# Kernel optimization log

Measured on AMD Instinct MI355X. Metric: run time of the kernel, lower is better.

## Reference

```python
import jax, jax.numpy as jnp
import numpy as np

N = 200000      # n_edges (1-simplices)
NNZ = 2000000   # nonzeros per sparse Laplacian
F_IN = 64       # num_edge_feats
F_H = 32        # f_size (hard-coded in FlowSAN)
F_OUT = 8       # output_size
G = 256         # number of graphs in batch
NEG_SLOPE = 0.2 # GAT LeakyReLU slope


def setup_inputs() -> dict:
    key = jax.random.key(0)
    ks = iter(jax.random.split(key, 64))

    def rn(shape, s=0.1):
        return jax.random.normal(next(ks), shape, dtype=jnp.float32) * s

    d = {"x1": jax.random.normal(next(ks), (N, F_IN), dtype=jnp.float32)}
    dims = [(F_IN, F_H), (F_H, F_H), (F_H, F_H), (F_H, F_OUT)]
    for i, (fi, fo) in enumerate(dims, 1):
        d[f"pW{i}"] = rn((fi, fo))                      # SANLayer.p_layer weight (bias=False)
        d[f"uW{i}"] = rn((fi, fo))                      # l_u GAT linear
        d[f"ua_s{i}"] = rn((fo,)); d[f"ua_d{i}"] = rn((fo,))  # l_u GAT attention vec halves
        d[f"dW{i}"] = rn((fi, fo))                      # l_d GAT linear
        d[f"da_s{i}"] = rn((fo,)); d[f"da_d{i}"] = rn((fo,))
    d["l1_idx"] = jax.random.randint(next(ks), (2, NNZ), 0, N, dtype=jnp.int32)
    d["l1_val"] = jax.random.normal(next(ks), (NNZ,), dtype=jnp.float32)
    d["lu_idx"] = jax.random.randint(next(ks), (2, NNZ), 0, N, dtype=jnp.int32)
    d["ld_idx"] = jax.random.randint(next(ks), (2, NNZ), 0, N, dtype=jnp.int32)
    d["batch1"] = jnp.sort(jax.random.randint(next(ks), (N,), 0, G, dtype=jnp.int32))
    return d


def _gat(x, W, a_s, a_d, idx):
    # GAT-style attention over the nonzero pattern of the sparse Laplacian
    h = x @ W                                   # [N, fo]
    row, col = idx[0], idx[1]
    e = jax.nn.leaky_relu(h[row] @ a_s + h[col] @ a_d, NEG_SLOPE)  # [nnz]
    e = e - jax.ops.segment_max(e, row, num_segments=N)[row]       # stable softmax
    w = jnp.exp(e)
    alpha = w / (jax.ops.segment_sum(w, row, num_segments=N)[row] + 1e-16)
    return jax.ops.segment_sum(alpha[:, None] * h[col], row, num_segments=N)


def _san(x, pW, uW, ua_s, ua_d, dW, da_s, da_d, l1_idx, l1_val, lu_idx, ld_idx):
    # p branch: torch.sparse.mm(L1, x @ pW)
    hp = x @ pW
    row, col = l1_idx[0], l1_idx[1]
    hp = jax.ops.segment_sum(l1_val[:, None] * hp[col], row, num_segments=N)
    hu = _gat(x, uW, ua_s, ua_d, lu_idx)
    hd = _gat(x, dW, da_s, da_d, ld_idx)
    return hu + hd + hp


def reference(x1,
              pW1, uW1, ua_s1, ua_d1, dW1, da_s1, da_d1,
              pW2, uW2, ua_s2, ua_d2, dW2, da_s2, da_d2,
              pW3, uW3, ua_s3, ua_d3, dW3, da_s3, da_d3,
              pW4, uW4, ua_s4, ua_d4, dW4, da_s4, da_d4,
              l1_idx, l1_val, lu_idx, ld_idx, batch1):
    layers = [
        (pW1, uW1, ua_s1, ua_d1, dW1, da_s1, da_d1),
        (pW2, uW2, ua_s2, ua_d2, dW2, da_s2, da_d2),
        (pW3, uW3, ua_s3, ua_d3, dW3, da_s3, da_d3),
        (pW4, uW4, ua_s4, ua_d4, dW4, da_s4, da_d4),
    ]
    x = x1
    for p in layers:
        x = jax.nn.relu(_san(x, *p, l1_idx, l1_val, lu_idx, ld_idx))
    # global_mean_pool(|x|, batch1)
    cnt = jax.ops.segment_sum(jnp.ones((N,), jnp.float32), batch1, num_segments=G)
    pooled = jax.ops.segment_sum(jnp.abs(x), batch1, num_segments=G) / jnp.maximum(cnt, 1.0)[:, None]
    return jax.nn.softmax(pooled, axis=1)
```

## Files before the change

### kernel.cpp

```cpp
#include <hip/hip_runtime.h>
#include <cmath>


#define N_    200000
#define NNZ_  2000000
#define G_    256


__global__ __launch_bounds__(256) void hist_k(const int* __restrict__ lu, const int* __restrict__ ld,
                                              const int* __restrict__ l1, int* __restrict__ deg,
                                              int* __restrict__ tick) {
    int i = blockIdx.x * 256 + threadIdx.x;
    if (i >= NNZ_ / 4) return;
    int e = i * 4;
    int4 ru = *reinterpret_cast<const int4*>(lu + e);
    int4 rd = *reinterpret_cast<const int4*>(ld + e);
    int4 rl = *reinterpret_cast<const int4*>(l1 + e);
    int4 t;
    t.x = atomicAdd(&deg[ru.x], 1);
    t.y = atomicAdd(&deg[ru.y], 1);
    t.z = atomicAdd(&deg[ru.z], 1);
    t.w = atomicAdd(&deg[ru.w], 1);
    *reinterpret_cast<int4*>(tick + e) = t;
    t.x = atomicAdd(&deg[N_ + rd.x], 1);
    t.y = atomicAdd(&deg[N_ + rd.y], 1);
    t.z = atomicAdd(&deg[N_ + rd.z], 1);
    t.w = atomicAdd(&deg[N_ + rd.w], 1);
    *reinterpret_cast<int4*>(tick + NNZ_ + e) = t;
    t.x = atomicAdd(&deg[2 * N_ + rl.x], 1);
    t.y = atomicAdd(&deg[2 * N_ + rl.y], 1);
    t.z = atomicAdd(&deg[2 * N_ + rl.z], 1);
    t.w = atomicAdd(&deg[2 * N_ + rl.w], 1);
    *reinterpret_cast<int4*>(tick + 2 * NNZ_ + e) = t;
}

__global__ __launch_bounds__(256) void scan1_k(const int* __restrict__ in, int* __restrict__ out,
                                               int* __restrict__ bsum, int n) {
    __shared__ int lds[256];
    int tid = threadIdx.x;
    int base = blockIdx.x * 1024 + tid * 4;
    int v0 = (base + 0 < n) ? in[base + 0] : 0;
    int v1 = (base + 1 < n) ? in[base + 1] : 0;
    int v2 = (base + 2 < n) ? in[base + 2] : 0;
    int v3 = (base + 3 < n) ? in[base + 3] : 0;
    int s = v0 + v1 + v2 + v3;
    lds[tid] = s;
    __syncthreads();
    for (int off = 1; off < 256; off <<= 1) {
        int t = (tid >= off) ? lds[tid - off] : 0;
        __syncthreads();
        lds[tid] += t;
        __syncthreads();
    }
    int excl = lds[tid] - s;
    if (base + 0 < n) out[base + 0] = excl;
    if (base + 1 < n) out[base + 1] = excl + v0;
    if (base + 2 < n) out[base + 2] = excl + v0 + v1;
    if (base + 3 < n) out[base + 3] = excl + v0 + v1 + v2;
    if (tid == 255) bsum[blockIdx.x] = lds[255];
}

__global__ __launch_bounds__(256) void scan2_k(int* __restrict__ bsum, int nb, int* __restrict__ total_out) {
    __shared__ int lds[256];
    __shared__ int run_s;
    int tid = threadIdx.x;
    if (tid == 0) run_s = 0;
    __syncthreads();
    for (int c0 = 0; c0 < nb; c0 += 256) {
        int i = c0 + tid;
        int s = (i < nb) ? bsum[i] : 0;
        lds[tid] = s;
        __syncthreads();
        for (int off = 1; off < 256; off <<= 1) {
            int t = (tid >= off) ? lds[tid - off] : 0;
            __syncthreads();
            lds[tid] += t;
            __syncthreads();
        }
        int run = run_s;
        if (i < nb) bsum[i] = run + lds[tid] - s;
        __syncthreads();
        if (tid == 0) run_s = run + lds[255];
        __syncthreads();
    }
    if (tid == 0 && total_out) *total_out = run_s;
}

__global__ __launch_bounds__(256) void scan3_k(int* __restrict__ out, const int* __restrict__ bsum, int n) {
    int add = bsum[blockIdx.x];
    int base = blockIdx.x * 1024 + threadIdx.x * 4;
    #pragma unroll
    for (int k = 0; k < 4; ++k)
        if (base + k < n) out[base + k] += add;
}

__global__ __launch_bounds__(256) void scatter_k(const int* __restrict__ lu, const int* __restrict__ ld,
                                                 const int* __restrict__ l1, const float* __restrict__ l1v,
                                                 const int* __restrict__ rptr, const int* __restrict__ tick,
                                                 int* __restrict__ cols, float* __restrict__ vcsr) {
    int i = blockIdx.x * 256 + threadIdx.x;
    if (i >= NNZ_ / 4) return;
    int e = i * 4;
    {
        int4 r = *reinterpret_cast<const int4*>(lu + e);
        int4 c = *reinterpret_cast<const int4*>(lu + NNZ_ + e);
        int4 t = *reinterpret_cast<const int4*>(tick + e);
        __builtin_nontemporal_store(c.x, &cols[rptr[r.x] + t.x]);
        __builtin_nontemporal_store(c.y, &cols[rptr[r.y] + t.y]);
        __builtin_nontemporal_store(c.z, &cols[rptr[r.z] + t.z]);
        __builtin_nontemporal_store(c.w, &cols[rptr[r.w] + t.w]);
    }
    {
        int4 r = *reinterpret_cast<const int4*>(ld + e);
        int4 c = *reinterpret_cast<const int4*>(ld + NNZ_ + e);
        int4 t = *reinterpret_cast<const int4*>(tick + NNZ_ + e);
        __builtin_nontemporal_store(c.x, &cols[rptr[N_ + r.x] + t.x]);
        __builtin_nontemporal_store(c.y, &cols[rptr[N_ + r.y] + t.y]);
        __builtin_nontemporal_store(c.z, &cols[rptr[N_ + r.z] + t.z]);
        __builtin_nontemporal_store(c.w, &cols[rptr[N_ + r.w] + t.w]);
    }
    {
        int4 r = *reinterpret_cast<const int4*>(l1 + e);
        int4 c = *reinterpret_cast<const int4*>(l1 + NNZ_ + e);
        int4 t = *reinterpret_cast<const int4*>(tick + 2 * NNZ_ + e);
        float4 v = *reinterpret_cast<const float4*>(l1v + e);
        int p0 = rptr[2 * N_ + r.x] + t.x;
        int p1 = rptr[2 * N_ + r.y] + t.y;
        int p2 = rptr[2 * N_ + r.z] + t.z;
        int p3 = rptr[2 * N_ + r.w] + t.w;
        __builtin_nontemporal_store(c.x, &cols[p0]);
        __builtin_nontemporal_store(c.y, &cols[p1]);
        __builtin_nontemporal_store(c.z, &cols[p2]);
        __builtin_nontemporal_store(c.w, &cols[p3]);
        __builtin_nontemporal_store(v.x, &vcsr[p0 - 2 * NNZ_]);
        __builtin_nontemporal_store(v.y, &vcsr[p1 - 2 * NNZ_]);
        __builtin_nontemporal_store(v.z, &vcsr[p2 - 2 * NNZ_]);
        __builtin_nontemporal_store(v.w, &vcsr[p3 - 2 * NNZ_]);
    }
}


template <int FI, int FO>
__global__ __launch_bounds__(256) void gemm3_k(const float* __restrict__ x,
                                               const float* __restrict__ uW, const float* __restrict__ uas,
                                               const float* __restrict__ uad,
                                               const float* __restrict__ dW, const float* __restrict__ das,
                                               const float* __restrict__ dad,
                                               const float* __restrict__ pW,
                                               float* __restrict__ HU, float* __restrict__ HD,
                                               float* __restrict__ HP,
                                               float* __restrict__ ssu, float* __restrict__ sdu,
                                               float* __restrict__ ssd, float* __restrict__ sdd) {
    constexpr int ROWS = 256 / FO;
    constexpr int XS = FI + 1;
    __shared__ float Wu[FI * FO], Wd[FI * FO], Wp[FI * FO];
    __shared__ float xs[ROWS * XS];
    int tid = threadIdx.x;
    for (int i = tid; i < FI * FO; i += 256) {
        Wu[i] = uW[i];
        Wd[i] = dW[i];
        Wp[i] = pW[i];
    }
    int row0 = blockIdx.x * ROWS;
    for (int i = tid; i < ROWS * FI; i += 256) {
        int r = i / FI, k = i - r * FI;
        int gr = row0 + r;
        xs[r * XS + k] = (gr < N_) ? x[(size_t)gr * FI + k] : 0.f;
    }
    __syncthreads();
    int r = tid / FO, j = tid - (tid / FO) * FO;
    int grow = row0 + r;
    float au = 0.f, ad = 0.f, ap = 0.f;
    #pragma unroll
    for (int k = 0; k < FI; ++k) {
        float xv = xs[r * XS + k];
        au = fmaf(xv, Wu[k * FO + j], au);
        ad = fmaf(xv, Wd[k * FO + j], ad);
        ap = fmaf(xv, Wp[k * FO + j], ap);
    }
    if (grow < N_) {
        HU[(size_t)grow * FO + j] = au;
        HD[(size_t)grow * FO + j] = ad;
        HP[(size_t)grow * FO + j] = ap;
    }
    float vsu = au * uas[j], vdu = au * uad[j];
    float vsd = ad * das[j], vdd = ad * dad[j];
    #pragma unroll
    for (int m = FO / 2; m >= 1; m >>= 1) {
        vsu += __shfl_xor(vsu, m, FO);
        vdu += __shfl_xor(vdu, m, FO);
        vsd += __shfl_xor(vsd, m, FO);
        vdd += __shfl_xor(vdd, m, FO);
    }
    if (j == 0 && grow < N_) {
        ssu[grow] = vsu; sdu[grow] = vdu;
        ssd[grow] = vsd; sdd[grow] = vdd;
    }
}


template <int FO, bool GAT>
__device__ __forceinline__ void edge_loop(const int* __restrict__ cols, const float* __restrict__ sdv,
                                          const float* __restrict__ vals, const float* __restrict__ H,
                                          int b, int e, int lane, float s_row, int vbase,
                                          float& ax, float& ay, float& az, float& aw, float& z) {
    int p = b;
    for (; p + 4 <= e; p += 4) {
        int c0 = cols[p], c1 = cols[p + 1], c2 = cols[p + 2], c3 = cols[p + 3];
        const float4 h0 = *reinterpret_cast<const float4*>(H + (size_t)c0 * FO + lane * 4);
        const float4 h1 = *reinterpret_cast<const float4*>(H + (size_t)c1 * FO + lane * 4);
        const float4 h2 = *reinterpret_cast<const float4*>(H + (size_t)c2 * FO + lane * 4);
        const float4 h3 = *reinterpret_cast<const float4*>(H + (size_t)c3 * FO + lane * 4);
        float w0, w1, w2, w3;
        if constexpr (GAT) {
            float g0 = s_row + sdv[c0];
            float g1 = s_row + sdv[c1];
            float g2 = s_row + sdv[c2];
            float g3 = s_row + sdv[c3];
            g0 = g0 > 0.f ? g0 : 0.2f * g0;
            g1 = g1 > 0.f ? g1 : 0.2f * g1;
            g2 = g2 > 0.f ? g2 : 0.2f * g2;
            g3 = g3 > 0.f ? g3 : 0.2f * g3;
            w0 = __expf(g0); w1 = __expf(g1); w2 = __expf(g2); w3 = __expf(g3);
            z += (w0 + w1) + (w2 + w3);
        } else {
            w0 = vals[p - vbase];
            w1 = vals[p - vbase + 1];
            w2 = vals[p - vbase + 2];
            w3 = vals[p - vbase + 3];
        }
        ax = fmaf(w0, h0.x, ax); ay = fmaf(w0, h0.y, ay);
        az = fmaf(w0, h0.z, az); aw = fmaf(w0, h0.w, aw);
        ax = fmaf(w1, h1.x, ax); ay = fmaf(w1, h1.y, ay);
        az = fmaf(w1, h1.z, az); aw = fmaf(w1, h1.w, aw);
        ax = fmaf(w2, h2.x, ax); ay = fmaf(w2, h2.y, ay);
        az = fmaf(w2, h2.z, az); aw = fmaf(w2, h2.w, aw);
        ax = fmaf(w3, h3.x, ax); ay = fmaf(w3, h3.y, ay);
        az = fmaf(w3, h3.z, az); aw = fmaf(w3, h3.w, aw);
    }
    for (; p < e; ++p) {
        int c = cols[p];
        const float4 hv = *reinterpret_cast<const float4*>(H + (size_t)c * FO + lane * 4);
        float wv;
        if constexpr (GAT) {
            float g = s_row + sdv[c];
            g = g > 0.f ? g : 0.2f * g;
            wv = __expf(g);
            z += wv;
        } else {
            wv = vals[p - vbase];
        }
        ax = fmaf(wv, hv.x, ax); ay = fmaf(wv, hv.y, ay);
        az = fmaf(wv, hv.z, az); aw = fmaf(wv, hv.w, aw);
    }
}

template <int FO>
__global__ __launch_bounds__(256) void gather3_k(const int* __restrict__ rptr, const int* __restrict__ cols,
                                                 const float* __restrict__ vcsr,
                                                 const float* __restrict__ HU, const float* __restrict__ HD,
                                                 const float* __restrict__ HP,
                                                 const float* __restrict__ ssu, const float* __restrict__ sdu,
                                                 const float* __restrict__ ssd, const float* __restrict__ sdd,
                                                 float* __restrict__ xout) {
    constexpr int LPR = FO / 4;
    constexpr int RPB = 256 / LPR;
    int tid = threadIdx.x;
    int lane = tid % LPR;
    int r = blockIdx.x * RPB + tid / LPR;
    if (r >= N_) return;
    float ox, oy, oz, ow;
    {
        float ax = 0.f, ay = 0.f, az = 0.f, aw = 0.f, z = 0.f;
        edge_loop<FO, true>(cols, sdu, nullptr, HU, rptr[r], rptr[r + 1], lane, ssu[r], 0,
                            ax, ay, az, aw, z);
        float inv = 1.f / (z + 1e-16f);
        ox = ax * inv; oy = ay * inv; oz = az * inv; ow = aw * inv;
    }
    {
        float ax = 0.f, ay = 0.f, az = 0.f, aw = 0.f, z = 0.f;
        edge_loop<FO, true>(cols, sdd, nullptr, HD, rptr[N_ + r], rptr[N_ + r + 1], lane, ssd[r], 0,
                            ax, ay, az, aw, z);
        float inv = 1.f / (z + 1e-16f);
        ox = fmaf(ax, inv, ox); oy = fmaf(ay, inv, oy);
        oz = fmaf(az, inv, oz); ow = fmaf(aw, inv, ow);
    }
    {
        float ax = 0.f, ay = 0.f, az = 0.f, aw = 0.f, z = 0.f;
        edge_loop<FO, false>(cols, nullptr, vcsr, HP, rptr[2 * N_ + r], rptr[2 * N_ + r + 1], lane,
                             0.f, 2 * NNZ_, ax, ay, az, aw, z);
        ox += ax; oy += ay; oz += az; ow += aw;
    }
    ox = fmaxf(ox, 0.f); oy = fmaxf(oy, 0.f);
    oz = fmaxf(oz, 0.f); ow = fmaxf(ow, 0.f);
    *reinterpret_cast<float4*>(xout + (size_t)r * FO + lane * 4) = make_float4(ox, oy, oz, ow);
}


__global__ __launch_bounds__(256) void pool_k(const float* __restrict__ x, const int* __restrict__ batch,
                                              float* __restrict__ out) {
    int g = blockIdx.x;
    __shared__ float part[256];
    __shared__ int sse[2];
    if (threadIdx.x < 2) {
        int target = g + threadIdx.x;
        int lo = 0, hi = N_;
        while (lo < hi) {
            int mid = (lo + hi) >> 1;
            if (batch[mid] < target) lo = mid + 1; else hi = mid;
        }
        sse[threadIdx.x] = lo;
    }
    __syncthreads();
    int s = sse[0], e = sse[1];
    int f = threadIdx.x % 8;
    float acc = 0.f;
    for (int i = s + threadIdx.x / 8; i < e; i += 32) acc += fabsf(x[(size_t)i * 8 + f]);
    part[threadIdx.x] = acc;
    __syncthreads();
    if (threadIdx.x < 8) {
        float t = 0.f;
        #pragma unroll
        for (int k = 0; k < 32; ++k) t += part[k * 8 + f];
        float cnt = (float)(e - s);
        part[f] = t / fmaxf(cnt, 1.0f);
    }
    __syncthreads();
    if (threadIdx.x == 0) {
        float m = part[0];
        for (int j = 1; j < 8; ++j) m = fmaxf(m, part[j]);
        float zs = 0.f;
        float ex[8];
        for (int j = 0; j < 8; ++j) { ex[j] = __expf(part[j] - m); zs += ex[j]; }
        for (int j = 0; j < 8; ++j) out[g * 8 + j] = ex[j] / zs;
    }
}


template <int FI, int FO>
static void run_layer(const float* xin, float* xout, const float* const* W,
                      float* HU, float* HD, float* HP,
                      float* SSU, float* SDU, float* SSD, float* SDD,
                      const int* PTR, const int* COLS, const float* VCSR, hipStream_t stream) {
    constexpr int ROWS = 256 / FO;
    constexpr int RPB = 256 / (FO / 4);
    gemm3_k<FI, FO><<<(N_ + ROWS - 1) / ROWS, 256, 0, stream>>>(
        xin, W[1], W[2], W[3], W[4], W[5], W[6], W[0],
        HU, HD, HP, SSU, SDU, SSD, SDD);
    gather3_k<FO><<<(N_ + RPB - 1) / RPB, 256, 0, stream>>>(
        PTR, COLS, VCSR, HU, HD, HP, SSU, SDU, SSD, SDD, xout);
}

extern "C" void kernel_launch(void* const* d_in, const int* in_sizes, int n_in, void* d_out,
                              int out_size, void* d_ws, size_t ws_size, hipStream_t stream) {
    (void)in_sizes; (void)n_in; (void)out_size; (void)ws_size;
    const float* x1     = (const float*)d_in[0];
    const int*   l1_idx = (const int*)d_in[29];
    const float* l1_val = (const float*)d_in[30];
    const int*   lu_idx = (const int*)d_in[31];
    const int*   ld_idx = (const int*)d_in[32];
    const int*   batch1 = (const int*)d_in[33];
    float* out = (float*)d_out;

    char* w = (char*)d_ws;
    size_t off = 0;
    auto alloc = [&](size_t bytes) -> char* {
        char* p = w + off;
        off = (off + bytes + 255) & ~(size_t)255;
        return p;
    };
    float* X    = (float*)alloc((size_t)N_ * 32 * 4);
    float* HU   = (float*)alloc((size_t)N_ * 32 * 4);
    float* HD   = (float*)alloc((size_t)N_ * 32 * 4);
    float* HP   = (float*)alloc((size_t)N_ * 32 * 4);
    float* SSU  = (float*)alloc((size_t)N_ * 4);
    float* SDU  = (float*)alloc((size_t)N_ * 4);
    float* SSD  = (float*)alloc((size_t)N_ * 4);
    float* SDD  = (float*)alloc((size_t)N_ * 4);
    int*   PTR  = (int*)alloc((size_t)(3 * N_ + 1) * 4);
    int*   DEG  = (int*)alloc((size_t)3 * N_ * 4);
    int*   BSUM = (int*)alloc((size_t)1024 * 4);
    int*   TICK = (int*)alloc((size_t)3 * NNZ_ * 4);
    int*   COLS = (int*)alloc((size_t)3 * NNZ_ * 4);
    float* VCSR = (float*)alloc((size_t)NNZ_ * 4);

    hipMemsetAsync(DEG, 0, (size_t)3 * N_ * 4, stream);
    int qbl = (NNZ_ / 4 + 255) / 256;
    hist_k<<<qbl, 256, 0, stream>>>(lu_idx, ld_idx, l1_idx, DEG, TICK);
    int n3 = 3 * N_;
    int nb = (n3 + 1023) / 1024;
    scan1_k<<<nb, 256, 0, stream>>>(DEG, PTR, BSUM, n3);
    scan2_k<<<1, 256, 0, stream>>>(BSUM, nb, PTR + n3);
    scan3_k<<<nb, 256, 0, stream>>>(PTR, BSUM, n3);
    scatter_k<<<qbl, 256, 0, stream>>>(lu_idx, ld_idx, l1_idx, l1_val, PTR, TICK, COLS, VCSR);

    const float* W0[7] = {(const float*)d_in[1], (const float*)d_in[2], (const float*)d_in[3],
                          (const float*)d_in[4], (const float*)d_in[5], (const float*)d_in[6],
                          (const float*)d_in[7]};
    const float* W1[7] = {(const float*)d_in[8],  (const float*)d_in[9],  (const float*)d_in[10],
                          (const float*)d_in[11], (const float*)d_in[12], (const float*)d_in[13],
                          (const float*)d_in[14]};
    const float* W2[7] = {(const float*)d_in[15], (const float*)d_in[16], (const float*)d_in[17],
                          (const float*)d_in[18], (const float*)d_in[19], (const float*)d_in[20],
                          (const float*)d_in[21]};
    const float* W3[7] = {(const float*)d_in[22], (const float*)d_in[23], (const float*)d_in[24],
                          (const float*)d_in[25], (const float*)d_in[26], (const float*)d_in[27],
                          (const float*)d_in[28]};

    run_layer<64, 32>(x1, X, W0, HU, HD, HP, SSU, SDU, SSD, SDD, PTR, COLS, VCSR, stream);
    run_layer<32, 32>(X, X, W1, HU, HD, HP, SSU, SDU, SSD, SDD, PTR, COLS, VCSR, stream);
    run_layer<32, 32>(X, X, W2, HU, HD, HP, SSU, SDU, SSD, SDD, PTR, COLS, VCSR, stream);
    run_layer<32, 8>(X, X, W3, HU, HD, HP, SSU, SDU, SSD, SDD, PTR, COLS, VCSR, stream);

    pool_k<<<G_, 256, 0, stream>>>(X, batch1, out);
}
```

Baseline: 1.552 ms.

## Fuse CSR scatter with layer-1 GEMM and split gather rows across two teams

```diff
diff --git a/kernel.cpp b/kernel.cpp
--- a/kernel.cpp
+++ b/kernel.cpp
@@ -94,48 +94,102 @@
         if (base + k < n) out[base + k] += add;
 }
 
-__global__ __launch_bounds__(256) void scatter_k(const int* __restrict__ lu, const int* __restrict__ ld,
-                                                 const int* __restrict__ l1, const float* __restrict__ l1v,
-                                                 const int* __restrict__ rptr, const int* __restrict__ tick,
-                                                 int* __restrict__ cols, float* __restrict__ vcsr) {
-    int i = blockIdx.x * 256 + threadIdx.x;
-    if (i >= NNZ_ / 4) return;
-    int e = i * 4;
-    {
-        int4 r = *reinterpret_cast<const int4*>(lu + e);
-        int4 c = *reinterpret_cast<const int4*>(lu + NNZ_ + e);
-        int4 t = *reinterpret_cast<const int4*>(tick + e);
-        __builtin_nontemporal_store(c.x, &cols[rptr[r.x] + t.x]);
-        __builtin_nontemporal_store(c.y, &cols[rptr[r.y] + t.y]);
-        __builtin_nontemporal_store(c.z, &cols[rptr[r.z] + t.z]);
-        __builtin_nontemporal_store(c.w, &cols[rptr[r.w] + t.w]);
-    }
-    {
-        int4 r = *reinterpret_cast<const int4*>(ld + e);
-        int4 c = *reinterpret_cast<const int4*>(ld + NNZ_ + e);
-        int4 t = *reinterpret_cast<const int4*>(tick + NNZ_ + e);
-        __builtin_nontemporal_store(c.x, &cols[rptr[N_ + r.x] + t.x]);
-        __builtin_nontemporal_store(c.y, &cols[rptr[N_ + r.y] + t.y]);
-        __builtin_nontemporal_store(c.z, &cols[rptr[N_ + r.z] + t.z]);
-        __builtin_nontemporal_store(c.w, &cols[rptr[N_ + r.w] + t.w]);
-    }
-    {
-        int4 r = *reinterpret_cast<const int4*>(l1 + e);
-        int4 c = *reinterpret_cast<const int4*>(l1 + NNZ_ + e);
-        int4 t = *reinterpret_cast<const int4*>(tick + 2 * NNZ_ + e);
+
+template <int FI, int FO, int SCB>
+__global__ __launch_bounds__(256) void scat_gemm_k(
+    const int* __restrict__ lu, const int* __restrict__ ld, const int* __restrict__ l1,
+    const float* __restrict__ l1v, const int* __restrict__ rptr, const int* __restrict__ tick,
+    int* __restrict__ cols, float* __restrict__ vcsr,
+    const float* __restrict__ x,
+    const float* __restrict__ uW, const float* __restrict__ uas, const float* __restrict__ uad,
+    const float* __restrict__ dW, const float* __restrict__ das, const float* __restrict__ dad,
+    const float* __restrict__ pW,
+    float* __restrict__ HU, float* __restrict__ HD, float* __restrict__ HP,
+    float* __restrict__ ssu, float* __restrict__ sdu,
+    float* __restrict__ ssd, float* __restrict__ sdd) {
+    if (blockIdx.x < SCB) {
+        int i = blockIdx.x * 256 + threadIdx.x;
+        if (i >= NNZ_ / 4) return;
+        int e = i * 4;
+        int4 ru = *reinterpret_cast<const int4*>(lu + e);
+        int4 rd = *reinterpret_cast<const int4*>(ld + e);
+        int4 rl = *reinterpret_cast<const int4*>(l1 + e);
+        int4 cu = *reinterpret_cast<const int4*>(lu + NNZ_ + e);
+        int4 cd = *reinterpret_cast<const int4*>(ld + NNZ_ + e);
+        int4 cl = *reinterpret_cast<const int4*>(l1 + NNZ_ + e);
+        int4 tu = *reinterpret_cast<const int4*>(tick + e);
+        int4 td = *reinterpret_cast<const int4*>(tick + NNZ_ + e);
+        int4 tl = *reinterpret_cast<const int4*>(tick + 2 * NNZ_ + e);
         float4 v = *reinterpret_cast<const float4*>(l1v + e);
-        int p0 = rptr[2 * N_ + r.x] + t.x;
-        int p1 = rptr[2 * N_ + r.y] + t.y;
-        int p2 = rptr[2 * N_ + r.z] + t.z;
-        int p3 = rptr[2 * N_ + r.w] + t.w;
-        __builtin_nontemporal_store(c.x, &cols[p0]);
-        __builtin_nontemporal_store(c.y, &cols[p1]);
-        __builtin_nontemporal_store(c.z, &cols[p2]);
-        __builtin_nontemporal_store(c.w, &cols[p3]);
-        __builtin_nontemporal_store(v.x, &vcsr[p0 - 2 * NNZ_]);
-        __builtin_nontemporal_store(v.y, &vcsr[p1 - 2 * NNZ_]);
-        __builtin_nontemporal_store(v.z, &vcsr[p2 - 2 * NNZ_]);
-        __builtin_nontemporal_store(v.w, &vcsr[p3 - 2 * NNZ_]);
+        int pu0 = rptr[ru.x] + tu.x, pu1 = rptr[ru.y] + tu.y;
+        int pu2 = rptr[ru.z] + tu.z, pu3 = rptr[ru.w] + tu.w;
+        int pd0 = rptr[N_ + rd.x] + td.x, pd1 = rptr[N_ + rd.y] + td.y;
+        int pd2 = rptr[N_ + rd.z] + td.z, pd3 = rptr[N_ + rd.w] + td.w;
+        int pl0 = rptr[2 * N_ + rl.x] + tl.x, pl1 = rptr[2 * N_ + rl.y] + tl.y;
+        int pl2 = rptr[2 * N_ + rl.z] + tl.z, pl3 = rptr[2 * N_ + rl.w] + tl.w;
+        __builtin_nontemporal_store(cu.x, &cols[pu0]);
+        __builtin_nontemporal_store(cu.y, &cols[pu1]);
+        __builtin_nontemporal_store(cu.z, &cols[pu2]);
+        __builtin_nontemporal_store(cu.w, &cols[pu3]);
+        __builtin_nontemporal_store(cd.x, &cols[pd0]);
+        __builtin_nontemporal_store(cd.y, &cols[pd1]);
+        __builtin_nontemporal_store(cd.z, &cols[pd2]);
+        __builtin_nontemporal_store(cd.w, &cols[pd3]);
+        __builtin_nontemporal_store(cl.x, &cols[pl0]);
+        __builtin_nontemporal_store(cl.y, &cols[pl1]);
+        __builtin_nontemporal_store(cl.z, &cols[pl2]);
+        __builtin_nontemporal_store(cl.w, &cols[pl3]);
+        __builtin_nontemporal_store(v.x, &vcsr[pl0 - 2 * NNZ_]);
+        __builtin_nontemporal_store(v.y, &vcsr[pl1 - 2 * NNZ_]);
+        __builtin_nontemporal_store(v.z, &vcsr[pl2 - 2 * NNZ_]);
+        __builtin_nontemporal_store(v.w, &vcsr[pl3 - 2 * NNZ_]);
+        return;
+    }
+    int bid = blockIdx.x - SCB;
+    constexpr int ROWS = 256 / FO;
+    constexpr int XS = FI + 1;
+    __shared__ float Wu[FI * FO], Wd[FI * FO], Wp[FI * FO];
+    __shared__ float xs[ROWS * XS];
+    int tid = threadIdx.x;
+    for (int i = tid; i < FI * FO; i += 256) {
+        Wu[i] = uW[i];
+        Wd[i] = dW[i];
+        Wp[i] = pW[i];
+    }
+    int row0 = bid * ROWS;
+    for (int i = tid; i < ROWS * FI; i += 256) {
+        int r = i / FI, k = i - r * FI;
+        int gr = row0 + r;
+        xs[r * XS + k] = (gr < N_) ? x[(size_t)gr * FI + k] : 0.f;
+    }
+    __syncthreads();
+    int r = tid / FO, j = tid - (tid / FO) * FO;
+    int grow = row0 + r;
+    float au = 0.f, ad = 0.f, ap = 0.f;
+    #pragma unroll
+    for (int k = 0; k < FI; ++k) {
+        float xv = xs[r * XS + k];
+        au = fmaf(xv, Wu[k * FO + j], au);
+        ad = fmaf(xv, Wd[k * FO + j], ad);
+        ap = fmaf(xv, Wp[k * FO + j], ap);
+    }
+    if (grow < N_) {
+        HU[(size_t)grow * FO + j] = au;
+        HD[(size_t)grow * FO + j] = ad;
+        HP[(size_t)grow * FO + j] = ap;
+    }
+    float vsu = au * uas[j], vdu = au * uad[j];
+    float vsd = ad * das[j], vdd = ad * dad[j];
+    #pragma unroll
+    for (int m = FO / 2; m >= 1; m >>= 1) {
+        vsu += __shfl_xor(vsu, m, FO);
+        vdu += __shfl_xor(vdu, m, FO);
+        vsd += __shfl_xor(vsd, m, FO);
+        vdd += __shfl_xor(vdd, m, FO);
+    }
+    if (j == 0 && grow < N_) {
+        ssu[grow] = vsu; sdu[grow] = vdu;
+        ssd[grow] = vsd; sdd[grow] = vdd;
     }
 }
 
@@ -204,9 +258,11 @@
                                           const float* __restrict__ vals, const float* __restrict__ H,
                                           int b, int e, int lane, float s_row, int vbase,
                                           float& ax, float& ay, float& az, float& aw, float& z) {
-    int p = b;
-    for (; p + 4 <= e; p += 4) {
-        int c0 = cols[p], c1 = cols[p + 1], c2 = cols[p + 2], c3 = cols[p + 3];
+    for (int p = b; p < e; p += 4) {
+        int q1 = p + 1 < e ? p + 1 : e - 1;
+        int q2 = p + 2 < e ? p + 2 : e - 1;
+        int q3 = p + 3 < e ? p + 3 : e - 1;
+        int c0 = cols[p], c1 = cols[q1], c2 = cols[q2], c3 = cols[q3];
         const float4 h0 = *reinterpret_cast<const float4*>(H + (size_t)c0 * FO + lane * 4);
         const float4 h1 = *reinterpret_cast<const float4*>(H + (size_t)c1 * FO + lane * 4);
         const float4 h2 = *reinterpret_cast<const float4*>(H + (size_t)c2 * FO + lane * 4);
@@ -221,13 +277,16 @@
             g1 = g1 > 0.f ? g1 : 0.2f * g1;
             g2 = g2 > 0.f ? g2 : 0.2f * g2;
             g3 = g3 > 0.f ? g3 : 0.2f * g3;
-            w0 = __expf(g0); w1 = __expf(g1); w2 = __expf(g2); w3 = __expf(g3);
+            w0 = __expf(g0);
+            w1 = p + 1 < e ? __expf(g1) : 0.f;
+            w2 = p + 2 < e ? __expf(g2) : 0.f;
+            w3 = p + 3 < e ? __expf(g3) : 0.f;
             z += (w0 + w1) + (w2 + w3);
         } else {
             w0 = vals[p - vbase];
-            w1 = vals[p - vbase + 1];
-            w2 = vals[p - vbase + 2];
-            w3 = vals[p - vbase + 3];
+            w1 = p + 1 < e ? vals[q1 - vbase] : 0.f;
+            w2 = p + 2 < e ? vals[q2 - vbase] : 0.f;
+            w3 = p + 3 < e ? vals[q3 - vbase] : 0.f;
         }
         ax = fmaf(w0, h0.x, ax); ay = fmaf(w0, h0.y, ay);
         az = fmaf(w0, h0.z, az); aw = fmaf(w0, h0.w, aw);
@@ -238,24 +297,9 @@
         ax = fmaf(w3, h3.x, ax); ay = fmaf(w3, h3.y, ay);
         az = fmaf(w3, h3.z, az); aw = fmaf(w3, h3.w, aw);
     }
-    for (; p < e; ++p) {
-        int c = cols[p];
-        const float4 hv = *reinterpret_cast<const float4*>(H + (size_t)c * FO + lane * 4);
-        float wv;
-        if constexpr (GAT) {
-            float g = s_row + sdv[c];
-            g = g > 0.f ? g : 0.2f * g;
-            wv = __expf(g);
-            z += wv;
-        } else {
-            wv = vals[p - vbase];
-        }
-        ax = fmaf(wv, hv.x, ax); ay = fmaf(wv, hv.y, ay);
-        az = fmaf(wv, hv.z, az); aw = fmaf(wv, hv.w, aw);
-    }
-}
-
-template <int FO>
+}
+
+template <int FO, int TEAMS>
 __global__ __launch_bounds__(256) void gather3_k(const int* __restrict__ rptr, const int* __restrict__ cols,
                                                  const float* __restrict__ vcsr,
                                                  const float* __restrict__ HU, const float* __restrict__ HD,
@@ -264,36 +308,57 @@
                                                  const float* __restrict__ ssd, const float* __restrict__ sdd,
                                                  float* __restrict__ xout) {
     constexpr int LPR = FO / 4;
-    constexpr int RPB = 256 / LPR;
+    constexpr int TPR = LPR * TEAMS;
+    constexpr int RPB = 256 / TPR;
     int tid = threadIdx.x;
-    int lane = tid % LPR;
-    int r = blockIdx.x * RPB + tid / LPR;
+    int lane = tid & (LPR - 1);
+    int team = (tid / LPR) & (TEAMS - 1);
+    int r = blockIdx.x * RPB + tid / TPR;
     if (r >= N_) return;
-    float ox, oy, oz, ow;
+    float ox = 0.f, oy = 0.f, oz = 0.f, ow = 0.f;
+
+    auto branch = [&](const float* H, const float* sdv, const float* vals, int base, int vbase,
+                      bool gat, float s_row, float& bx, float& by, float& bz, float& bw, float& z) {
+        int b0 = rptr[base + r], e0 = rptr[base + r + 1];
+        int half = (e0 - b0) >> 1;
+        int tb = team == 0 ? b0 : b0 + half;
+        int te = team == 0 ? b0 + half : e0;
+        if (tb < te) {
+            if (gat)
+                edge_loop<FO, true>(cols, sdv, nullptr, H, tb, te, lane, s_row, 0, bx, by, bz, bw, z);
+            else
+                edge_loop<FO, false>(cols, nullptr, vals, H, tb, te, lane, 0.f, vbase, bx, by, bz, bw, z);
+        }
+        bx += __shfl_xor(bx, LPR, TPR);
+        by += __shfl_xor(by, LPR, TPR);
+        bz += __shfl_xor(bz, LPR, TPR);
+        bw += __shfl_xor(bw, LPR, TPR);
+        if (gat) z += __shfl_xor(z, LPR, TPR);
+    };
+
     {
         float ax = 0.f, ay = 0.f, az = 0.f, aw = 0.f, z = 0.f;
-        edge_loop<FO, true>(cols, sdu, nullptr, HU, rptr[r], rptr[r + 1], lane, ssu[r], 0,
-                            ax, ay, az, aw, z);
+        branch(HU, sdu, nullptr, 0, 0, true, ssu[r], ax, ay, az, aw, z);
         float inv = 1.f / (z + 1e-16f);
         ox = ax * inv; oy = ay * inv; oz = az * inv; ow = aw * inv;
     }
     {
         float ax = 0.f, ay = 0.f, az = 0.f, aw = 0.f, z = 0.f;
-        edge_loop<FO, true>(cols, sdd, nullptr, HD, rptr[N_ + r], rptr[N_ + r + 1], lane, ssd[r], 0,
-                            ax, ay, az, aw, z);
+        branch(HD, sdd, nullptr, N_, 0, true, ssd[r], ax, ay, az, aw, z);
         float inv = 1.f / (z + 1e-16f);
         ox = fmaf(ax, inv, ox); oy = fmaf(ay, inv, oy);
         oz = fmaf(az, inv, oz); ow = fmaf(aw, inv, ow);
     }
     {
         float ax = 0.f, ay = 0.f, az = 0.f, aw = 0.f, z = 0.f;
-        edge_loop<FO, false>(cols, nullptr, vcsr, HP, rptr[2 * N_ + r], rptr[2 * N_ + r + 1], lane,
-                             0.f, 2 * NNZ_, ax, ay, az, aw, z);
+        branch(HP, nullptr, vcsr, 2 * N_, 2 * NNZ_, false, 0.f, ax, ay, az, aw, z);
         ox += ax; oy += ay; oz += az; ow += aw;
     }
-    ox = fmaxf(ox, 0.f); oy = fmaxf(oy, 0.f);
-    oz = fmaxf(oz, 0.f); ow = fmaxf(ow, 0.f);
-    *reinterpret_cast<float4*>(xout + (size_t)r * FO + lane * 4) = make_float4(ox, oy, oz, ow);
+    if (team == 0) {
+        ox = fmaxf(ox, 0.f); oy = fmaxf(oy, 0.f);
+        oz = fmaxf(oz, 0.f); ow = fmaxf(ow, 0.f);
+        *reinterpret_cast<float4*>(xout + (size_t)r * FO + lane * 4) = make_float4(ox, oy, oz, ow);
+    }
 }
 
 
@@ -343,11 +408,11 @@
                       float* SSU, float* SDU, float* SSD, float* SDD,
                       const int* PTR, const int* COLS, const float* VCSR, hipStream_t stream) {
     constexpr int ROWS = 256 / FO;
-    constexpr int RPB = 256 / (FO / 4);
+    constexpr int RPB = 256 / ((FO / 4) * 2);
     gemm3_k<FI, FO><<<(N_ + ROWS - 1) / ROWS, 256, 0, stream>>>(
         xin, W[1], W[2], W[3], W[4], W[5], W[6], W[0],
         HU, HD, HP, SSU, SDU, SSD, SDD);
-    gather3_k<FO><<<(N_ + RPB - 1) / RPB, 256, 0, stream>>>(
+    gather3_k<FO, 2><<<(N_ + RPB - 1) / RPB, 256, 0, stream>>>(
         PTR, COLS, VCSR, HU, HD, HP, SSU, SDU, SSD, SDD, xout);
 }
 
@@ -384,16 +449,6 @@
     int*   COLS = (int*)alloc((size_t)3 * NNZ_ * 4);
     float* VCSR = (float*)alloc((size_t)NNZ_ * 4);
 
-    hipMemsetAsync(DEG, 0, (size_t)3 * N_ * 4, stream);
-    int qbl = (NNZ_ / 4 + 255) / 256;
-    hist_k<<<qbl, 256, 0, stream>>>(lu_idx, ld_idx, l1_idx, DEG, TICK);
-    int n3 = 3 * N_;
-    int nb = (n3 + 1023) / 1024;
-    scan1_k<<<nb, 256, 0, stream>>>(DEG, PTR, BSUM, n3);
-    scan2_k<<<1, 256, 0, stream>>>(BSUM, nb, PTR + n3);
-    scan3_k<<<nb, 256, 0, stream>>>(PTR, BSUM, n3);
-    scatter_k<<<qbl, 256, 0, stream>>>(lu_idx, ld_idx, l1_idx, l1_val, PTR, TICK, COLS, VCSR);
-
     const float* W0[7] = {(const float*)d_in[1], (const float*)d_in[2], (const float*)d_in[3],
                           (const float*)d_in[4], (const float*)d_in[5], (const float*)d_in[6],
                           (const float*)d_in[7]};
@@ -407,7 +462,29 @@
                           (const float*)d_in[25], (const float*)d_in[26], (const float*)d_in[27],
                           (const float*)d_in[28]};
 
-    run_layer<64, 32>(x1, X, W0, HU, HD, HP, SSU, SDU, SSD, SDD, PTR, COLS, VCSR, stream);
+    hipMemsetAsync(DEG, 0, (size_t)3 * N_ * 4, stream);
+    constexpr int QBL = (NNZ_ / 4 + 255) / 256;
+    hist_k<<<QBL, 256, 0, stream>>>(lu_idx, ld_idx, l1_idx, DEG, TICK);
+    int n3 = 3 * N_;
+    int nb = (n3 + 1023) / 1024;
+    scan1_k<<<nb, 256, 0, stream>>>(DEG, PTR, BSUM, n3);
+    scan2_k<<<1, 256, 0, stream>>>(BSUM, nb, PTR + n3);
+    scan3_k<<<nb, 256, 0, stream>>>(PTR, BSUM, n3);
+
+    {
+        constexpr int ROWS = 256 / 32;
+        int gemmb = (N_ + ROWS - 1) / ROWS;
+        scat_gemm_k<64, 32, QBL><<<QBL + gemmb, 256, 0, stream>>>(
+            lu_idx, ld_idx, l1_idx, l1_val, PTR, TICK, COLS, VCSR,
+            x1, W0[1], W0[2], W0[3], W0[4], W0[5], W0[6], W0[0],
+            HU, HD, HP, SSU, SDU, SSD, SDD);
+    }
+    {
+        constexpr int RPB = 256 / ((32 / 4) * 2);
+        gather3_k<32, 2><<<(N_ + RPB - 1) / RPB, 256, 0, stream>>>(
+            PTR, COLS, VCSR, HU, HD, HP, SSU, SDU, SSD, SDD, X);
+    }
+
     run_layer<32, 32>(X, X, W1, HU, HD, HP, SSU, SDU, SSD, SDD, PTR, COLS, VCSR, stream);
     run_layer<32, 32>(X, X, W2, HU, HD, HP, SSU, SDU, SSD, SDD, PTR, COLS, VCSR, stream);
     run_layer<32, 8>(X, X, W3, HU, HD, HP, SSU, SDU, SSD, SDD, PTR, COLS, VCSR, stream);
```

Measured after the change: 1.544 ms. Within noise of the previous version (-0.5%).
